# Performance work log

Hardware: AMD Instinct MI355X
Metric: run time of the kernel (lower is better)

Reference implementation:

```python
import jax, jax.numpy as jnp
import numpy as np
from jax import lax


def _forward(matrix_states, candidate_actions, candidate_actions_features,
             conv_w, conv_b, wq, bq, wk, bk, wv, bv, wo, bo,
             mlp_w1, mlp_b1, mlp_w2, mlp_b2):
    # --- CNN feature extractor on each state matrix (batched, not looped) ---
    x = matrix_states[:, None, :, :]  # [M,1,H,W]
    c = lax.conv_general_dilated(
        x, conv_w, window_strides=(1, 1), padding=[(1, 1), (1, 1)],
        dimension_numbers=('NCHW', 'OIHW', 'NCHW'))
    c = jax.nn.relu(c + conv_b[None, :, None, None])  # [M,16,H+1,W+1]
    M, C, Hc, Wc = c.shape
    # AdaptiveAvgPool2d((2,2)) with even spatial dims -> exact half bins
    pooled = c.reshape(M, C, 2, Hc // 2, 2, Wc // 2).mean(axis=(3, 5))  # [M,16,2,2]
    state_feature = pooled.reshape(1, M * C * 4)  # torch cat of [1,64] feats -> [1, M*64]

    # --- gather candidate action features ---
    af = candidate_actions_features[candidate_actions]  # [A,F]
    A, F = af.shape

    # --- single-head self-attention over actions ---
    Q = af @ wq + bq  # [A,F]
    K = af @ wk + bk
    V = af @ wv + bv
    energy = (Q @ K.T) / jnp.sqrt(jnp.asarray(F, af.dtype))  # [A,A]
    attn = jax.nn.softmax(energy, axis=-1)
    out = attn @ V          # [A,F]
    out = out @ wo + bo     # fc_out

    # --- MLP scoring: concat(state_feature, action_feat) per action, batched ---
    st = jnp.broadcast_to(state_feature, (A, state_feature.shape[1]))  # [A,S]
    combined = jnp.concatenate([st, out], axis=1)  # [A, S+F]
    h = jax.nn.relu(combined @ mlp_w1 + mlp_b1)    # [A,16]
    scores = (h @ mlp_w2 + mlp_b2)[:, 0]           # [A]
    return jax.nn.softmax(scores, axis=0)


def setup_inputs() -> dict:
    key = jax.random.key(0)
    ks = jax.random.split(key, 12)
    M, H, W = 3, 255, 255
    A, Vtab, F = 8192, 16384, 16
    S = M * 64                # state feature dim = 192
    Dc = S + F                # combined_dim = 208
    f32 = jnp.float32

    def n(k, shape, scale):
        return jax.random.normal(k, shape, dtype=f32) * scale

    return {
        'matrix_states': jax.random.normal(ks[0], (M, H, W), dtype=f32),
        'candidate_actions': jax.random.randint(ks[1], (A,), 0, Vtab),
        'candidate_actions_features': jax.random.normal(ks[2], (Vtab, F), dtype=f32),
        'conv_w': n(ks[3], (16, 1, 2, 2), 0.5),
        'conv_b': jnp.zeros((16,), f32),
        'wq': n(ks[4], (F, F), 0.25), 'bq': jnp.zeros((F,), f32),
        'wk': n(ks[5], (F, F), 0.25), 'bk': jnp.zeros((F,), f32),
        'wv': n(ks[6], (F, F), 0.25), 'bv': jnp.zeros((F,), f32),
        'wo': n(ks[7], (F, F), 0.25), 'bo': jnp.zeros((F,), f32),
        'mlp_w1': n(ks[8], (Dc, 16), 0.07), 'mlp_b1': jnp.zeros((16,), f32),
        'mlp_w2': n(ks[9], (16, 1), 0.25), 'mlp_b2': jnp.zeros((1,), f32),
    }


def reference(matrix_states, candidate_actions, candidate_actions_features,
              conv_w, conv_b, wq, bq, wk, bk, wv, bv, wo, bo,
              mlp_w1, mlp_b1, mlp_w2, mlp_b2):
    return _forward(matrix_states, candidate_actions, candidate_actions_features,
                    conv_w, conv_b, wq, bq, wk, bk, wv, bv, wo, bo,
                    mlp_w1, mlp_b1, mlp_w2, mlp_b2)
```

## Files before the change

### kernel.cpp

```cpp
#include <hip/hip_runtime.h>
#include <hip/hip_bf16.h>

#define A_N 8192
#define LOG2E 1.44269504f

typedef __attribute__((ext_vector_type(8))) short short8v;
typedef __attribute__((ext_vector_type(4))) float f32x4;
typedef __attribute__((ext_vector_type(4))) int   i32x4;

__device__ inline short f2bf(float x) {
  unsigned u = __builtin_bit_cast(unsigned, x);
  unsigned r = (u + 0x7FFFu + ((u >> 16) & 1u)) >> 16;
  return (short)r;
}
__device__ inline float fexp2(float x) {
#if __has_builtin(__builtin_amdgcn_exp2f)
  return __builtin_amdgcn_exp2f(x);
#else
  return exp2f(x);
#endif
}
__device__ inline unsigned cvtpk2(float lo, float hi) {
  float2 t; t.x = lo; t.y = hi;
  __hip_bfloat162 h = __float22bfloat162_rn(t);
  unsigned r; __builtin_memcpy(&r, &h, 4);
  return r;
}

__global__ __launch_bounds__(256) void fused_pre(
    const float* __restrict__ x, const float* __restrict__ cw,
    const float* __restrict__ cb, float* __restrict__ sfp,
    const int* __restrict__ act, const float* __restrict__ feat,
    const float* __restrict__ wq, const float* __restrict__ bq,
    const float* __restrict__ wk, const float* __restrict__ bk,
    const float* __restrict__ wv, const float* __restrict__ bv,
    const float* __restrict__ wo,
    short* __restrict__ Qo, short* __restrict__ Ko, short* __restrict__ V2S,
    int* __restrict__ counter) {
  __shared__ float swq[256], swk[256], swv[256], swo[256];
  __shared__ float sbq[16], sbk[16], sbv[16];
  __shared__ float red[4];
  int tid = threadIdx.x;
  if (blockIdx.x == 0 && tid == 0) *counter = 0;
  if (blockIdx.x < 1536) {
    int bid2 = blockIdx.x;
    int u    = bid2 & 7;
    int base = bid2 >> 3;
    int b  = base & 1;
    int a  = (base >> 1) & 1;
    int ch = (base >> 2) & 15;
    int m  = base >> 6;
    float w00 = cw[ch*4+0], w01 = cw[ch*4+1], w10 = cw[ch*4+2], w11 = cw[ch*4+3];
    float bias = cb[ch];
    const float* xm = x + (size_t)m * 255 * 255;
    float sum = 0.f;
    #pragma unroll
    for (int it = 0; it < 8; ++it) {
      int p = u*2048 + it*256 + tid;
      int i = a*128 + (p >> 7);
      int j = b*128 + (p & 127);
      float x00 = (i >= 1 && j >= 1)   ? xm[(i-1)*255 + (j-1)] : 0.f;
      float x01 = (i >= 1 && j <= 254) ? xm[(i-1)*255 + j]     : 0.f;
      float x10 = (i <= 254 && j >= 1) ? xm[i*255 + (j-1)]     : 0.f;
      float x11 = (i <= 254 && j <= 254) ? xm[i*255 + j]       : 0.f;
      float v = fmaf(x00,w00, fmaf(x01,w01, fmaf(x10,w10, fmaf(x11,w11, bias))));
      sum += fmaxf(v, 0.f);
    }
    for (int o = 32; o; o >>= 1) sum += __shfl_down(sum, o, 64);
    int wid = tid >> 6, lane = tid & 63;
    if (lane == 0) red[wid] = sum;
    __syncthreads();
    if (tid == 0) sfp[bid2] = red[0]+red[1]+red[2]+red[3];
  } else {
    swq[tid] = wq[tid]; swk[tid] = wk[tid]; swv[tid] = wv[tid]; swo[tid] = wo[tid];
    if (tid < 16) { sbq[tid] = bq[tid]; sbk[tid] = bk[tid]; sbv[tid] = bv[tid]; }
    __syncthreads();
    int row = (blockIdx.x - 1536) * 256 + tid;
    int idx = act[row];
    const float4* f4 = (const float4*)(feat + (size_t)idx * 16);
    float4 a0 = f4[0], a1 = f4[1], a2 = f4[2], a3 = f4[3];
    float af[16] = {a0.x,a0.y,a0.z,a0.w, a1.x,a1.y,a1.z,a1.w,
                    a2.x,a2.y,a2.z,a2.w, a3.x,a3.y,a3.z,a3.w};
    float q[16], k[16], v[16];
    #pragma unroll
    for (int kk = 0; kk < 16; ++kk) {
      float aq = sbq[kk], ak = sbk[kk], av = sbv[kk];
      #pragma unroll
      for (int f = 0; f < 16; ++f) {
        aq = fmaf(af[f], swq[f*16+kk], aq);
        ak = fmaf(af[f], swk[f*16+kk], ak);
        av = fmaf(af[f], swv[f*16+kk], av);
      }
      q[kk] = aq; k[kk] = ak; v[kk] = av;
    }
    const float qs = 0.25f * LOG2E;
    int s  = row >> 5;
    int jj = row & 31;
    int hi = jj >> 4;
    int m2 = jj & 15;
    int gsw = m2 >> 2;
    int rsw = m2 & 3;
    size_t vbase = (size_t)s * 512 + (size_t)gsw * 128 + hi * 4 + rsw;
    #pragma unroll
    for (int kk = 0; kk < 16; ++kk) {
      float a = 0.f;
      #pragma unroll
      for (int f = 0; f < 16; ++f) a = fmaf(v[f], swo[f*16+kk], a);
      V2S[vbase + (size_t)kk * 8] = f2bf(a);
      Qo[(size_t)row*16 + kk] = f2bf(q[kk] * qs);
      Ko[(size_t)row*16 + kk] = f2bf(k[kk]);
    }
  }
}

__global__ __launch_bounds__(1024) void attn_score(
    const short* __restrict__ Qb, const short* __restrict__ Kb,
    const short* __restrict__ V2S, const float* __restrict__ sfp,
    const float* __restrict__ w1, const float* __restrict__ b1,
    const float* __restrict__ bo, const float* __restrict__ w2,
    float* __restrict__ scores, int* __restrict__ counter,
    float* __restrict__ outp) {
  __shared__ float sacc[16][32][16];
  __shared__ float sl[16][32];
  __shared__ float sw1[256];
  __shared__ float scvp[16][16];
  __shared__ float scv[16], sw2s[16];
  __shared__ float red2[16];
  __shared__ float sbc2[2];
  __shared__ int slastS;
  int tid = threadIdx.x;
  if (tid < 256) {
    sw1[tid] = w1[192*16 + tid];
    int c4 = tid >> 4, kq = tid & 15;
    float acc = (c4 == 0) ? b1[kq] : 0.f;
    #pragma unroll
    for (int si = 0; si < 12; ++si) {
      int s = c4*12 + si;
      const float* pp = sfp + s*8;
      float sv = ((pp[0]+pp[1])+(pp[2]+pp[3])) + ((pp[4]+pp[5])+(pp[6]+pp[7]));
      acc = fmaf(sv * (1.0f/16384.0f), w1[s*16+kq], acc);
    }
    if (c4 == 1) {
      #pragma unroll
      for (int f = 0; f < 16; ++f) acc = fmaf(bo[f], w1[(192+f)*16+kq], acc);
    }
    scvp[c4][kq] = acc;
  }
  if (tid < 16) sw2s[tid] = w2[tid];
  int w = tid >> 6, lane = tid & 63;
  int g = lane >> 4, fi = lane & 15;
  int i0 = blockIdx.x * 32;

  short8v z8 = {};
  short8v qfa = z8, qfb = z8;
  if (g < 2) {
    qfa = *(const short8v*)(Qb + (size_t)(i0 + fi)*16 + g*8);
    qfb = *(const short8v*)(Qb + (size_t)(i0 + 16 + fi)*16 + g*8);
  }
  const short* kp = Kb + (size_t)(w*512 + fi)*16 + g*8;
  const short* vp = V2S + (size_t)(w*1024 + lane)*8;

  f32x4 acca = {0.f,0.f,0.f,0.f}, accb = {0.f,0.f,0.f,0.f};
  float lsa = 0.f, lsb = 0.f;

  short8v k0c = *(const short8v*)kp;
  short8v k1c = *(const short8v*)(kp + 256);
  i32x4  vvc = *(const i32x4*)(vp);
  short8v k0x = *(const short8v*)(kp + 512);
  short8v k1x = *(const short8v*)(kp + 768);
  i32x4  vvx = *(const i32x4*)(vp + 512);

  #pragma unroll 2
  for (int step = 0; step < 16; ++step) {
    short8v k0n = z8, k1n = z8; i32x4 vvn = {0,0,0,0};
    if (step < 14) {
      k0n = *(const short8v*)(kp + 1024);
      k1n = *(const short8v*)(kp + 1280);
      vvn = *(const i32x4*)(vp + 1024);
    }
    short8v vf = __builtin_bit_cast(short8v, vvc);
    f32x4 zero4 = {0.f,0.f,0.f,0.f};
    f32x4 e0a = __builtin_amdgcn_mfma_f32_16x16x32_bf16(k0c, qfa, zero4, 0, 0, 0);
    f32x4 e1a = __builtin_amdgcn_mfma_f32_16x16x32_bf16(k1c, qfa, zero4, 0, 0, 0);
    f32x4 e0b = __builtin_amdgcn_mfma_f32_16x16x32_bf16(k0c, qfb, zero4, 0, 0, 0);
    f32x4 e1b = __builtin_amdgcn_mfma_f32_16x16x32_bf16(k1c, qfb, zero4, 0, 0, 0);
    {
      float p0 = fexp2(e0a[0]), p1 = fexp2(e0a[1]), p2 = fexp2(e0a[2]), p3 = fexp2(e0a[3]);
      float p4 = fexp2(e1a[0]), p5 = fexp2(e1a[1]), p6 = fexp2(e1a[2]), p7 = fexp2(e1a[3]);
      lsa += ((p0+p1)+(p2+p3)) + ((p4+p5)+(p6+p7));
      i32x4 pk;
      pk[0] = (int)cvtpk2(p0, p1); pk[1] = (int)cvtpk2(p2, p3);
      pk[2] = (int)cvtpk2(p4, p5); pk[3] = (int)cvtpk2(p6, p7);
      acca = __builtin_amdgcn_mfma_f32_16x16x32_bf16(__builtin_bit_cast(short8v, pk), vf, acca, 0, 0, 0);
    }
    {
      float p0 = fexp2(e0b[0]), p1 = fexp2(e0b[1]), p2 = fexp2(e0b[2]), p3 = fexp2(e0b[3]);
      float p4 = fexp2(e1b[0]), p5 = fexp2(e1b[1]), p6 = fexp2(e1b[2]), p7 = fexp2(e1b[3]);
      lsb += ((p0+p1)+(p2+p3)) + ((p4+p5)+(p6+p7));
      i32x4 pk;
      pk[0] = (int)cvtpk2(p0, p1); pk[1] = (int)cvtpk2(p2, p3);
      pk[2] = (int)cvtpk2(p4, p5); pk[3] = (int)cvtpk2(p6, p7);
      accb = __builtin_amdgcn_mfma_f32_16x16x32_bf16(__builtin_bit_cast(short8v, pk), vf, accb, 0, 0, 0);
    }
    k0c = k0x; k1c = k1x; vvc = vvx;
    k0x = k0n; k1x = k1n; vvx = vvn;
    kp += 512;
    vp += 512;
  }
  lsa += __shfl_xor(lsa, 16, 64); lsa += __shfl_xor(lsa, 32, 64);
  lsb += __shfl_xor(lsb, 16, 64); lsb += __shfl_xor(lsb, 32, 64);
  #pragma unroll
  for (int r = 0; r < 4; ++r) {
    sacc[w][4*g + r][fi]      = acca[r];
    sacc[w][16 + 4*g + r][fi] = accb[r];
  }
  if (g == 0) { sl[w][fi] = lsa; sl[w][16 + fi] = lsb; }
  __syncthreads();
  if (tid < 512) {
    int i = tid >> 4, f = tid & 15;
    float o = 0.f, li = 0.f;
    #pragma unroll
    for (int wv = 0; wv < 16; ++wv) { o += sacc[wv][i][f]; li += sl[wv][i]; }
    sacc[0][i][f] = o / li;
  } else if (tid < 528) {
    int k = tid - 512;
    float s = 0.f;
    #pragma unroll
    for (int c = 0; c < 16; ++c) s += scvp[c][k];
    scv[k] = s;
  }
  __syncthreads();
  if (tid < 512) {
    int i = tid >> 4, k = tid & 15;
    float h = scv[k];
    #pragma unroll
    for (int f = 0; f < 16; ++f) h = fmaf(sacc[0][i][f], sw1[f*16+k], h);
    h = fmaxf(h, 0.f);
    float t = h * sw2s[k];
    t += __shfl_xor(t, 1, 64);
    t += __shfl_xor(t, 2, 64);
    t += __shfl_xor(t, 4, 64);
    t += __shfl_xor(t, 8, 64);
    if (k == 0)
      __hip_atomic_store(&scores[i0 + i], t, __ATOMIC_RELAXED, __HIP_MEMORY_SCOPE_AGENT);
  }
  __syncthreads();
  if (tid == 0)
    slastS = __hip_atomic_fetch_add(counter, 1, __ATOMIC_ACQ_REL, __HIP_MEMORY_SCOPE_AGENT);
  __syncthreads();
  if (slastS != (A_N/32) - 1) return;

  float sv[8];
  #pragma unroll
  for (int u = 0; u < 8; ++u)
    sv[u] = __hip_atomic_load(&scores[tid + u*1024], __ATOMIC_RELAXED, __HIP_MEMORY_SCOPE_AGENT);
  int lane2 = tid & 63, wid2 = tid >> 6;
  float m = -3.4e38f;
  #pragma unroll
  for (int u = 0; u < 8; ++u) m = fmaxf(m, sv[u]);
  for (int o = 32; o; o >>= 1) m = fmaxf(m, __shfl_down(m, o, 64));
  if (lane2 == 0) red2[wid2] = m;
  __syncthreads();
  if (tid == 0) {
    float mm = red2[0];
    for (int wv = 1; wv < 16; ++wv) mm = fmaxf(mm, red2[wv]);
    sbc2[0] = mm;
  }
  __syncthreads();
  float mx = sbc2[0];
  float s = 0.f;
  #pragma unroll
  for (int u = 0; u < 8; ++u) s += __expf(sv[u] - mx);
  for (int o = 32; o; o >>= 1) s += __shfl_down(s, o, 64);
  if (lane2 == 0) red2[wid2] = s;
  __syncthreads();
  if (tid == 0) {
    float ss = 0.f;
    for (int wv = 0; wv < 16; ++wv) ss += red2[wv];
    sbc2[1] = ss;
  }
  __syncthreads();
  float inv = 1.0f / sbc2[1];
  #pragma unroll
  for (int u = 0; u < 8; ++u)
    outp[tid + u*1024] = __expf(sv[u] - mx) * inv;
}

extern "C" void kernel_launch(void* const* d_in, const int* in_sizes, int n_in,
                              void* d_out, int out_size, void* d_ws, size_t ws_size,
                              hipStream_t stream) {
  const float* x      = (const float*)d_in[0];
  const int*   act    = (const int*)  d_in[1];
  const float* feat   = (const float*)d_in[2];
  const float* conv_w = (const float*)d_in[3];
  const float* conv_b = (const float*)d_in[4];
  const float* wq     = (const float*)d_in[5];
  const float* bq     = (const float*)d_in[6];
  const float* wk     = (const float*)d_in[7];
  const float* bk     = (const float*)d_in[8];
  const float* wv     = (const float*)d_in[9];
  const float* bv     = (const float*)d_in[10];
  const float* wo     = (const float*)d_in[11];
  const float* bo     = (const float*)d_in[12];
  const float* w1     = (const float*)d_in[13];
  const float* b1     = (const float*)d_in[14];
  const float* w2     = (const float*)d_in[15];

  char* wsb = (char*)d_ws;
  float* sfp    = (float*)(wsb);
  int*   ctr    = (int*)  (wsb + 8192);
  float* scores = (float*)(wsb + 16384);
  short* Qb     = (short*)(wsb + 65536);
  short* Kb     = (short*)(wsb + 65536 + 262144);
  short* V2S    = (short*)(wsb + 65536 + 524288);
  float* out    = (float*)d_out;

  fused_pre  <<<1568, 256, 0, stream>>>(x, conv_w, conv_b, sfp,
                                        act, feat, wq, bq, wk, bk, wv, bv, wo,
                                        Qb, Kb, V2S, ctr);
  attn_score <<<A_N/32, 1024, 0, stream>>>(Qb, Kb, V2S, sfp, w1, b1, bo, w2,
                                           scores, ctr, out);
}
```

Baseline: 36.40 us.

## Fuse preprocessing and attention kernels into one persistent kernel with grid barrier

Merges the conv/pool and QKV projection kernel into the attention-scoring kernel. A single launch of 256 blocks of 1024 threads does its share of the conv sums and projections, then waits at a software grid barrier built on an atomic counter before starting attention. The barrier and completion counters are zeroed with a memset before the launch. This removes one kernel launch and the gap between the two kernels, but it relies on all 256 blocks being resident at once (deadlock risk otherwise) and runs the preprocessing with fewer, larger blocks.

```diff
diff --git a/kernel.cpp b/kernel.cpp
--- a/kernel.cpp
+++ b/kernel.cpp
@@ -2,6 +2,7 @@
 #include <hip/hip_bf16.h>
 
 #define A_N 8192
+#define NBLK 256
 #define LOG2E 1.44269504f
 
 typedef __attribute__((ext_vector_type(8))) short short8v;
@@ -27,7 +28,7 @@
   return r;
 }
 
-__global__ __launch_bounds__(256) void fused_pre(
+__global__ __launch_bounds__(1024) void fused_all(
     const float* __restrict__ x, const float* __restrict__ cw,
     const float* __restrict__ cb, float* __restrict__ sfp,
     const int* __restrict__ act, const float* __restrict__ feat,
@@ -35,90 +36,10 @@
     const float* __restrict__ wk, const float* __restrict__ bk,
     const float* __restrict__ wv, const float* __restrict__ bv,
     const float* __restrict__ wo,
-    short* __restrict__ Qo, short* __restrict__ Ko, short* __restrict__ V2S,
-    int* __restrict__ counter) {
-  __shared__ float swq[256], swk[256], swv[256], swo[256];
-  __shared__ float sbq[16], sbk[16], sbv[16];
-  __shared__ float red[4];
-  int tid = threadIdx.x;
-  if (blockIdx.x == 0 && tid == 0) *counter = 0;
-  if (blockIdx.x < 1536) {
-    int bid2 = blockIdx.x;
-    int u    = bid2 & 7;
-    int base = bid2 >> 3;
-    int b  = base & 1;
-    int a  = (base >> 1) & 1;
-    int ch = (base >> 2) & 15;
-    int m  = base >> 6;
-    float w00 = cw[ch*4+0], w01 = cw[ch*4+1], w10 = cw[ch*4+2], w11 = cw[ch*4+3];
-    float bias = cb[ch];
-    const float* xm = x + (size_t)m * 255 * 255;
-    float sum = 0.f;
-    #pragma unroll
-    for (int it = 0; it < 8; ++it) {
-      int p = u*2048 + it*256 + tid;
-      int i = a*128 + (p >> 7);
-      int j = b*128 + (p & 127);
-      float x00 = (i >= 1 && j >= 1)   ? xm[(i-1)*255 + (j-1)] : 0.f;
-      float x01 = (i >= 1 && j <= 254) ? xm[(i-1)*255 + j]     : 0.f;
-      float x10 = (i <= 254 && j >= 1) ? xm[i*255 + (j-1)]     : 0.f;
-      float x11 = (i <= 254 && j <= 254) ? xm[i*255 + j]       : 0.f;
-      float v = fmaf(x00,w00, fmaf(x01,w01, fmaf(x10,w10, fmaf(x11,w11, bias))));
-      sum += fmaxf(v, 0.f);
-    }
-    for (int o = 32; o; o >>= 1) sum += __shfl_down(sum, o, 64);
-    int wid = tid >> 6, lane = tid & 63;
-    if (lane == 0) red[wid] = sum;
-    __syncthreads();
-    if (tid == 0) sfp[bid2] = red[0]+red[1]+red[2]+red[3];
-  } else {
-    swq[tid] = wq[tid]; swk[tid] = wk[tid]; swv[tid] = wv[tid]; swo[tid] = wo[tid];
-    if (tid < 16) { sbq[tid] = bq[tid]; sbk[tid] = bk[tid]; sbv[tid] = bv[tid]; }
-    __syncthreads();
-    int row = (blockIdx.x - 1536) * 256 + tid;
-    int idx = act[row];
-    const float4* f4 = (const float4*)(feat + (size_t)idx * 16);
-    float4 a0 = f4[0], a1 = f4[1], a2 = f4[2], a3 = f4[3];
-    float af[16] = {a0.x,a0.y,a0.z,a0.w, a1.x,a1.y,a1.z,a1.w,
-                    a2.x,a2.y,a2.z,a2.w, a3.x,a3.y,a3.z,a3.w};
-    float q[16], k[16], v[16];
-    #pragma unroll
-    for (int kk = 0; kk < 16; ++kk) {
-      float aq = sbq[kk], ak = sbk[kk], av = sbv[kk];
-      #pragma unroll
-      for (int f = 0; f < 16; ++f) {
-        aq = fmaf(af[f], swq[f*16+kk], aq);
-        ak = fmaf(af[f], swk[f*16+kk], ak);
-        av = fmaf(af[f], swv[f*16+kk], av);
-      }
-      q[kk] = aq; k[kk] = ak; v[kk] = av;
-    }
-    const float qs = 0.25f * LOG2E;
-    int s  = row >> 5;
-    int jj = row & 31;
-    int hi = jj >> 4;
-    int m2 = jj & 15;
-    int gsw = m2 >> 2;
-    int rsw = m2 & 3;
-    size_t vbase = (size_t)s * 512 + (size_t)gsw * 128 + hi * 4 + rsw;
-    #pragma unroll
-    for (int kk = 0; kk < 16; ++kk) {
-      float a = 0.f;
-      #pragma unroll
-      for (int f = 0; f < 16; ++f) a = fmaf(v[f], swo[f*16+kk], a);
-      V2S[vbase + (size_t)kk * 8] = f2bf(a);
-      Qo[(size_t)row*16 + kk] = f2bf(q[kk] * qs);
-      Ko[(size_t)row*16 + kk] = f2bf(k[kk]);
-    }
-  }
-}
-
-__global__ __launch_bounds__(1024) void attn_score(
-    const short* __restrict__ Qb, const short* __restrict__ Kb,
-    const short* __restrict__ V2S, const float* __restrict__ sfp,
+    short* __restrict__ Qb, short* __restrict__ Kb, short* __restrict__ V2S,
     const float* __restrict__ w1, const float* __restrict__ b1,
     const float* __restrict__ bo, const float* __restrict__ w2,
-    float* __restrict__ scores, int* __restrict__ counter,
+    float* __restrict__ scores, int* __restrict__ bar, int* __restrict__ ctr,
     float* __restrict__ outp) {
   __shared__ float sacc[16][32][16];
   __shared__ float sl[16][32];
@@ -127,8 +48,100 @@
   __shared__ float scv[16], sw2s[16];
   __shared__ float red2[16];
   __shared__ float sbc2[2];
+  __shared__ float sred[4][4];
+  __shared__ float vtmp[32][16];
   __shared__ int slastS;
   int tid = threadIdx.x;
+  int b = blockIdx.x;
+
+  {
+    int gq = tid >> 8;
+    int t256 = tid & 255;
+    int lane = tid & 63;
+    int wl = (tid >> 6) & 3;
+    #pragma unroll
+    for (int r = 0; r < 2; ++r) {
+      int sub = r*4 + gq;
+      int un = 6*b + sub;
+      float sum = 0.f;
+      if (sub < 6) {
+        int u = un & 7;
+        int base = un >> 3;
+        int bb = base & 1;
+        int aa = (base >> 1) & 1;
+        int ch = (base >> 2) & 15;
+        int m  = base >> 6;
+        float w00 = cw[ch*4+0], w01 = cw[ch*4+1], w10 = cw[ch*4+2], w11 = cw[ch*4+3];
+        float bias = cb[ch];
+        const float* xm = x + (size_t)m * 255 * 255;
+        #pragma unroll
+        for (int it = 0; it < 8; ++it) {
+          int p = u*2048 + it*256 + t256;
+          int i = aa*128 + (p >> 7);
+          int j = bb*128 + (p & 127);
+          float x00 = (i >= 1 && j >= 1)   ? xm[(i-1)*255 + (j-1)] : 0.f;
+          float x01 = (i >= 1 && j <= 254) ? xm[(i-1)*255 + j]     : 0.f;
+          float x10 = (i <= 254 && j >= 1) ? xm[i*255 + (j-1)]     : 0.f;
+          float x11 = (i <= 254 && j <= 254) ? xm[i*255 + j]       : 0.f;
+          float v = fmaf(x00,w00, fmaf(x01,w01, fmaf(x10,w10, fmaf(x11,w11, bias))));
+          sum += fmaxf(v, 0.f);
+        }
+        for (int o = 32; o; o >>= 1) sum += __shfl_down(sum, o, 64);
+      }
+      if (sub < 6 && lane == 0) sred[gq][wl] = sum;
+      __syncthreads();
+      if (sub < 6 && t256 == 0)
+        sfp[un] = sred[gq][0]+sred[gq][1]+sred[gq][2]+sred[gq][3];
+      __syncthreads();
+    }
+  }
+
+  {
+    int rowl = tid >> 4;
+    int kk = tid & 15;
+    float q = 0.f, k = 0.f, v = 0.f;
+    int row = b*32 + rowl;
+    if (tid < 512) {
+      int idx = act[row];
+      const float* af = feat + (size_t)idx * 16;
+      q = bq[kk]; k = bk[kk]; v = bv[kk];
+      #pragma unroll
+      for (int f = 0; f < 16; ++f) {
+        float a = af[f];
+        q = fmaf(a, wq[f*16+kk], q);
+        k = fmaf(a, wk[f*16+kk], k);
+        v = fmaf(a, wv[f*16+kk], v);
+      }
+      vtmp[rowl][kk] = v;
+    }
+    __syncthreads();
+    if (tid < 512) {
+      float a2 = 0.f;
+      #pragma unroll
+      for (int f = 0; f < 16; ++f) a2 = fmaf(vtmp[rowl][f], wo[f*16+kk], a2);
+      const float qs = 0.25f * LOG2E;
+      Qb[(size_t)row*16 + kk] = f2bf(q * qs);
+      Kb[(size_t)row*16 + kk] = f2bf(k);
+      int s  = row >> 5;
+      int jj = row & 31;
+      int hi = jj >> 4;
+      int m2 = jj & 15;
+      int gsw = m2 >> 2;
+      int rsw = m2 & 3;
+      V2S[(size_t)s*512 + (size_t)gsw*128 + hi*4 + rsw + (size_t)kk*8] = f2bf(a2);
+    }
+  }
+
+  __threadfence();
+  __syncthreads();
+  if (tid == 0) {
+    __hip_atomic_fetch_add(bar, 1, __ATOMIC_ACQ_REL, __HIP_MEMORY_SCOPE_AGENT);
+    while (__hip_atomic_load(bar, __ATOMIC_ACQUIRE, __HIP_MEMORY_SCOPE_AGENT) < NBLK) {
+      __builtin_amdgcn_s_sleep(1);
+    }
+  }
+  __syncthreads();
+
   if (tid < 256) {
     sw1[tid] = w1[192*16 + tid];
     int c4 = tid >> 4, kq = tid & 15;
@@ -149,7 +162,7 @@
   if (tid < 16) sw2s[tid] = w2[tid];
   int w = tid >> 6, lane = tid & 63;
   int g = lane >> 4, fi = lane & 15;
-  int i0 = blockIdx.x * 32;
+  int i0 = b * 32;
 
   short8v z8 = {};
   short8v qfa = z8, qfb = z8;
@@ -246,9 +259,9 @@
   }
   __syncthreads();
   if (tid == 0)
-    slastS = __hip_atomic_fetch_add(counter, 1, __ATOMIC_ACQ_REL, __HIP_MEMORY_SCOPE_AGENT);
-  __syncthreads();
-  if (slastS != (A_N/32) - 1) return;
+    slastS = __hip_atomic_fetch_add(ctr, 1, __ATOMIC_ACQ_REL, __HIP_MEMORY_SCOPE_AGENT);
+  __syncthreads();
+  if (slastS != NBLK - 1) return;
 
   float sv[8];
   #pragma unroll
@@ -308,16 +321,17 @@
 
   char* wsb = (char*)d_ws;
   float* sfp    = (float*)(wsb);
-  int*   ctr    = (int*)  (wsb + 8192);
+  int*   bar    = (int*)  (wsb + 8192);
+  int*   ctr    = (int*)  (wsb + 8448);
   float* scores = (float*)(wsb + 16384);
   short* Qb     = (short*)(wsb + 65536);
   short* Kb     = (short*)(wsb + 65536 + 262144);
   short* V2S    = (short*)(wsb + 65536 + 524288);
   float* out    = (float*)d_out;
 
-  fused_pre  <<<1568, 256, 0, stream>>>(x, conv_w, conv_b, sfp,
+  hipMemsetAsync(wsb + 8192, 0, 512, stream);
+  fused_all <<<NBLK, 1024, 0, stream>>>(x, conv_w, conv_b, sfp,
                                         act, feat, wq, bq, wk, bk, wv, bv, wo,
-                                        Qb, Kb, V2S, ctr);
-  attn_score <<<A_N/32, 1024, 0, stream>>>(Qb, Kb, V2S, sfp, w1, b1, bo, w2,
-                                           scores, ctr, out);
-}
+                                        Qb, Kb, V2S, w1, b1, bo, w2,
+                                        scores, bar, ctr, out);
+}
```

Measured after the change: 116.9 us. 221% more time.
